# Optimization experiments

Hardware: AMD Instinct MI355X
Metric: run time of the kernel (lower is better)

The kernel has to match this reference:

```python
import jax, jax.numpy as jnp
import numpy as np

B, S, E, D, M = 512, 64, 768, 256, 3  # batch, seq, encoder_dim, dim, num_modalities


def setup_inputs() -> dict:
    key = jax.random.key(0)
    ks = jax.random.split(key, 16)
    inp = {}
    for i in range(M):
        inp[f"latent{i}"] = jax.random.normal(ks[i], (B, S, E), dtype=jnp.float32)
        inp[f"Wp{i}"] = jax.random.normal(ks[3 + i], (D, E), dtype=jnp.float32) * (1.0 / np.sqrt(E))
        inp[f"bp{i}"] = jnp.zeros((D,), dtype=jnp.float32)
    inp["corr"] = jax.random.uniform(ks[7], (D, D), dtype=jnp.float32, minval=-0.1, maxval=0.1)
    F_in = 2 * D * (M - 1)  # 1024
    inp["Wb"] = jax.random.normal(ks[8], (64, F_in), dtype=jnp.float32) * (1.0 / np.sqrt(F_in))
    inp["bb"] = jnp.zeros((64,), dtype=jnp.float32)
    inp["gamma"] = jnp.ones((64,), dtype=jnp.float32)
    inp["beta"] = jnp.zeros((64,), dtype=jnp.float32)
    return inp


def _forward(latents, Wps, bps, corr, Wb, bb, gamma, beta):
    # project each modality: [B,S,E] -> [B,S,D]
    proj = [lat @ Wp.T + bp for lat, Wp, bp in zip(latents, Wps, bps)]
    anchor = proj[0]
    pairs = []
    for other in proj[1:]:
        # cc[b,i,j] = anchor[b,i,:] @ corr @ other[b,j,:]
        cc = jnp.einsum('bid,de,bje->bij', anchor, corr, other)
        a_att = jax.nn.softmax(cc, axis=1)   # softmax over anchor tokens
        o_att = jax.nn.softmax(cc, axis=2)   # softmax over other tokens (= softmax(cc^T, dim=1))
        att_anchor = jnp.einsum('bid,bij->bdj', anchor, a_att) + jnp.swapaxes(anchor, 1, 2)
        att_other = jnp.einsum('bjd,bij->bdi', other, o_att) + jnp.swapaxes(other, 1, 2)
        pairs.append(jnp.concatenate([att_anchor, att_other], axis=1))  # [B,2D,S]
    fused = jnp.concatenate(pairs, axis=1)          # [B, 2D(M-1), S]
    fused = jnp.swapaxes(fused, 1, 2)               # [B, S, 2D(M-1)]
    h = fused @ Wb.T + bb                           # [B, S, 64]
    mu = jnp.mean(h, axis=-1, keepdims=True)
    var = jnp.var(h, axis=-1, keepdims=True)
    h = (h - mu) / jnp.sqrt(var + 1e-5) * gamma + beta
    return jax.nn.relu(h)


def reference(latent0, latent1, latent2, Wp0, bp0, Wp1, bp1, Wp2, bp2, corr, Wb, bb, gamma, beta):
    return _forward([latent0, latent1, latent2], [Wp0, Wp1, Wp2], [bp0, bp1, bp2],
                    corr, Wb, bb, gamma, beta)
```

## Files before the change

### kernel.cpp

```cpp
#include <hip/hip_runtime.h>
#include <hip/hip_bf16.h>
#include <stdint.h>

#define Bsz 512
#define Ssz 64
#define Esz 768
#define Dsz 256
#define MROWS (Bsz * Ssz)
#define FIN 1024

typedef _Float16 f16;
typedef f16 f16x4 __attribute__((ext_vector_type(4)));
typedef f16 f16x8v __attribute__((ext_vector_type(8)));
typedef float f32x4 __attribute__((ext_vector_type(4)));

__device__ __forceinline__ void async_copy16(const void* g, void* l) {
    __builtin_amdgcn_global_load_lds((const __attribute__((address_space(1))) uint32_t*)g,
                                     (__attribute__((address_space(3))) uint32_t*)l, 16, 0, 0);
}

__global__ __launch_bounds__(256) void prep(const float* __restrict__ Wp0,
                                            const float* __restrict__ Wp1,
                                            const float* __restrict__ Wp2,
                                            const float* __restrict__ corr,
                                            const float* __restrict__ Wb,
                                            f16* __restrict__ Wph,
                                            f16* __restrict__ corrT,
                                            f16* __restrict__ Wbh) {
    const int t = blockIdx.x * 256 + threadIdx.x;
    if (t < 3 * 196608) {
        const int z = t / 196608, i = t % 196608;
        const float* W = (z == 0) ? Wp0 : (z == 1) ? Wp1 : Wp2;
        Wph[(size_t)z * 196608 + i] = (f16)W[i];
    }
    if (t < 65536) {
        const int d = t >> 8, e = t & 255;
        corrT[e * 256 + d] = (f16)corr[d * 256 + e];
        Wbh[t] = (f16)Wb[t];
    }
}

template <bool A_F16, bool BIAS>
__global__ __launch_bounds__(256) void mfma_gemm(
    const float* __restrict__ A32a, const float* __restrict__ A32b,
    const float* __restrict__ A32c, const f16* __restrict__ A16,
    const f16* __restrict__ Bh, const float* __restrict__ biasA,
    const float* __restrict__ biasB, const float* __restrict__ biasC,
    f16* __restrict__ Ch, int K) {
    constexpr int ABYTES = A_F16 ? 8192 : 16384;
    constexpr int BUF = ABYTES + 8192;
    __shared__ __align__(16) char smem[2 * BUF];

    const int tid = threadIdx.x;
    const int n0 = blockIdx.x * 128;
    const int m0 = blockIdx.y * 128;
    const int z = blockIdx.z;
    const float* A32 = (z == 0) ? A32a : (z == 1) ? A32b : A32c;
    const float* bias = (z == 0) ? biasA : (z == 1) ? biasB : biasC;
    const f16* Bz = Bh + (size_t)z * 256 * K;
    f16* Cz = Ch + (size_t)z * MROWS * 256;

    const int lane = tid & 63;
    const int w = tid >> 6;
    const int lr = lane & 15;
    const int lk = lane >> 4;
    const int ma = (w >> 1) * 4;
    const int nb = (w & 1) * 4;

    f32x4 acc[4][4];
#pragma unroll
    for (int i = 0; i < 4; i++)
#pragma unroll
        for (int j = 0; j < 4; j++) acc[i][j] = (f32x4){0.f, 0.f, 0.f, 0.f};

    auto stage = [&](int buf, int k0) {
        char* base = smem + buf * BUF;
#pragma unroll
        for (int i = 0; i < (A_F16 ? 2 : 4); i++) {
            const int Ub = (w * (A_F16 ? 2 : 4) + i) * 64;
            const int U = Ub + lane;
            if constexpr (A_F16) {
                const int row = U >> 2, u = (U & 3) ^ (row & 3);
                async_copy16(A16 + (size_t)(m0 + row) * K + k0 + u * 8, base + Ub * 16);
            } else {
                const int row = U >> 3, c = (U & 7) ^ (row & 7);
                async_copy16(A32 + (size_t)(m0 + row) * K + k0 + c * 4, base + Ub * 16);
            }
        }
#pragma unroll
        for (int i = 0; i < 2; i++) {
            const int Ub = (w * 2 + i) * 64;
            const int U = Ub + lane;
            const int row = U >> 2, u = (U & 3) ^ (row & 3);
            async_copy16(Bz + (size_t)(n0 + row) * K + k0 + u * 8, base + ABYTES + Ub * 16);
        }
    };

    stage(0, 0);
    int cur = 0;
    const int NT = K >> 5;
    for (int t = 0; t < NT; t++) {
        if (t + 1 < NT) {
            stage(cur ^ 1, (t + 1) << 5);
            if constexpr (A_F16) {
                asm volatile("s_waitcnt vmcnt(4)" ::: "memory");
            } else {
                asm volatile("s_waitcnt vmcnt(6)" ::: "memory");
            }
        } else {
            asm volatile("s_waitcnt vmcnt(0)" ::: "memory");
        }
        __builtin_amdgcn_sched_barrier(0);
        asm volatile("s_barrier" ::: "memory");
        __builtin_amdgcn_sched_barrier(0);

        const char* base = smem + cur * BUF;
        const f16* Af16L = (const f16*)base;
        const float* Af32L = (const float*)base;
        const f16* BfL = (const f16*)(base + ABYTES);
        f16x8v af[4], bf[4];
#pragma unroll
        for (int i = 0; i < 4; i++) {
            const int row = (ma + i) * 16 + lr;
            if constexpr (A_F16) {
                const int u = lk ^ (row & 3);
                af[i] = *(const f16x8v*)&Af16L[(row * 4 + u) * 8];
            } else {
                const int c0 = (2 * lk) ^ (row & 7);
                const int c1 = (2 * lk + 1) ^ (row & 7);
                const float4 v1 = *(const float4*)&Af32L[(row * 8 + c0) * 4];
                const float4 v2 = *(const float4*)&Af32L[(row * 8 + c1) * 4];
                f16x8v h;
                h[0] = (f16)v1.x; h[1] = (f16)v1.y; h[2] = (f16)v1.z; h[3] = (f16)v1.w;
                h[4] = (f16)v2.x; h[5] = (f16)v2.y; h[6] = (f16)v2.z; h[7] = (f16)v2.w;
                af[i] = h;
            }
        }
#pragma unroll
        for (int j = 0; j < 4; j++) {
            const int row = (nb + j) * 16 + lr;
            const int u = lk ^ (row & 3);
            bf[j] = *(const f16x8v*)&BfL[(row * 4 + u) * 8];
        }
#pragma unroll
        for (int i = 0; i < 4; i++)
#pragma unroll
            for (int j = 0; j < 4; j++)
                acc[i][j] = __builtin_amdgcn_mfma_f32_16x16x32_f16(af[i], bf[j], acc[i][j], 0, 0, 0);

        __builtin_amdgcn_sched_barrier(0);
        asm volatile("s_barrier" ::: "memory");
        cur ^= 1;
    }

    f16* Ce = (f16*)smem;
    const int cr = lane & 15, qr = lane >> 4;
    const int mwl = (w >> 1) * 64;
    const int nwl = (w & 1) * 64;
#pragma unroll
    for (int i = 0; i < 4; i++) {
#pragma unroll
        for (int j = 0; j < 4; j++) {
            const int col = nwl + j * 16 + cr;
            const float bv = BIAS ? bias[n0 + col] : 0.f;
#pragma unroll
            for (int r = 0; r < 4; r++) {
                const int row = mwl + i * 16 + qr * 4 + r;
                Ce[row * 128 + col] = (f16)(acc[i][j][r] + bv);
            }
        }
    }
    __syncthreads();
#pragma unroll
    for (int r = 0; r < 8; r++) {
        const int f = r * 256 + tid;
        const int row = f >> 4, c16 = f & 15;
        uint4 v = *(const uint4*)&Ce[row * 128 + c16 * 8];
        *(uint4*)(Cz + (size_t)(m0 + row) * 256 + n0 + c16 * 8) = v;
    }
}

__global__ __launch_bounds__(256) void cc_softmax(const f16* __restrict__ ac,
                                                  const f16* __restrict__ proj1,
                                                  const f16* __restrict__ proj2,
                                                  f16* __restrict__ aT,
                                                  f16* __restrict__ oP) {
    const int b = blockIdx.x, q = blockIdx.y;
    const f16* __restrict__ A = ac + (size_t)b * Ssz * Dsz;
    const f16* __restrict__ Bp = (q ? proj2 : proj1) + (size_t)b * Ssz * Dsz;
    __shared__ float sc[64][65];
    __shared__ float pm[4][64], ps[4][64], qm[4][64], qs[4][64];
    __shared__ float CM[64], CI[64], RM[64], RI[64];
    const int tid = threadIdx.x;
    const int lane = tid & 63, w = tid >> 6;
    const int lr = lane & 15;
    const int lk = lane >> 4;

    f32x4 acc[4];
#pragma unroll
    for (int j = 0; j < 4; j++) acc[j] = (f32x4){0.f, 0.f, 0.f, 0.f};

    const f16* __restrict__ Arow = A + (size_t)(w * 16 + lr) * Dsz + lk * 8;
    for (int ks = 0; ks < 8; ks++) {
        f16x8v af = *(const f16x8v*)(Arow + ks * 32);
        f16x8v bf[4];
#pragma unroll
        for (int j = 0; j < 4; j++)
            bf[j] = *(const f16x8v*)(Bp + (size_t)(j * 16 + lr) * Dsz + ks * 32 + lk * 8);
#pragma unroll
        for (int j = 0; j < 4; j++)
            acc[j] = __builtin_amdgcn_mfma_f32_16x16x32_f16(af, bf[j], acc[j], 0, 0, 0);
    }
#pragma unroll
    for (int j = 0; j < 4; j++)
#pragma unroll
        for (int r = 0; r < 4; r++) sc[w * 16 + lk * 4 + r][j * 16 + lr] = acc[j][r];
    __syncthreads();

    const int lid = tid & 63, qa = tid >> 6;
    float m1 = -1e30f, m2 = -1e30f;
#pragma unroll
    for (int it = 0; it < 16; it++) {
        m1 = fmaxf(m1, sc[qa * 16 + it][lid]);
        m2 = fmaxf(m2, sc[lid][qa * 16 + it]);
    }
    float s1 = 0.f, s2 = 0.f;
#pragma unroll
    for (int it = 0; it < 16; it++) {
        s1 += __expf(sc[qa * 16 + it][lid] - m1);
        s2 += __expf(sc[lid][qa * 16 + it] - m2);
    }
    pm[qa][lid] = m1; ps[qa][lid] = s1;
    qm[qa][lid] = m2; qs[qa][lid] = s2;
    __syncthreads();
    if (tid < 128) {
        const int x = tid & 63;
        const bool col = tid < 64;
        float M = -1e30f;
#pragma unroll
        for (int u = 0; u < 4; u++) M = fmaxf(M, col ? pm[u][x] : qm[u][x]);
        float S = 0.f;
#pragma unroll
        for (int u = 0; u < 4; u++)
            S += (col ? ps[u][x] : qs[u][x]) * __expf((col ? pm[u][x] : qm[u][x]) - M);
        if (col) { CM[x] = M; CI[x] = 1.f / S; }
        else     { RM[x] = M; RI[x] = 1.f / S; }
    }
    __syncthreads();
    f16* __restrict__ apT = aT + (size_t)(q * Bsz + b) * 4096;
    f16* __restrict__ opR = oP + (size_t)(q * Bsz + b) * 4096;
#pragma unroll
    for (int it = 0; it < 16; it++) {
        const int i = qa * 16 + it;
        opR[i * 64 + lid] = (f16)(__expf(sc[i][lid] - RM[i]) * RI[i]);
        apT[i * 64 + lid] = (f16)(__expf(sc[lid][i] - CM[i]) * CI[i]);
    }
}

__global__ __launch_bounds__(256) void fused_tail(const f16* __restrict__ proj,
                                                  const f16* __restrict__ Wbh,
                                                  const f16* __restrict__ aT,
                                                  const f16* __restrict__ oP,
                                                  const float* __restrict__ bb,
                                                  const float* __restrict__ gamma,
                                                  const float* __restrict__ beta,
                                                  float* __restrict__ out) {
    const int b = blockIdx.x;
    const int tid = threadIdx.x, lane = tid & 63, w = tid >> 6;
    const int lr = lane & 15, lk = lane >> 4;

    __shared__ __align__(16) f16 Gs[4][4096];

    {
        const int q = w >> 1, part = w & 1;
        const int z = part ? (1 + q) : 0;
        const f16* __restrict__ X = proj + ((size_t)z * MROWS + b * 64) * 256;
        const f16* __restrict__ Wc = Wbh + q * 512 + part * 256;
        f32x4 gacc[4][4];
#pragma unroll
        for (int i = 0; i < 4; i++)
#pragma unroll
            for (int j = 0; j < 4; j++) gacc[i][j] = (f32x4){0.f, 0.f, 0.f, 0.f};
        for (int ks = 0; ks < 8; ks++) {
            f16x8v af[4], bf[4];
#pragma unroll
            for (int mi = 0; mi < 4; mi++)
                af[mi] = *(const f16x8v*)(Wc + (size_t)(mi * 16 + lr) * FIN + ks * 32 + lk * 8);
#pragma unroll
            for (int nj = 0; nj < 4; nj++)
                bf[nj] = *(const f16x8v*)(X + (size_t)(nj * 16 + lr) * 256 + ks * 32 + lk * 8);
#pragma unroll
            for (int mi = 0; mi < 4; mi++)
#pragma unroll
                for (int nj = 0; nj < 4; nj++)
                    gacc[mi][nj] = __builtin_amdgcn_mfma_f32_16x16x32_f16(af[mi], bf[nj], gacc[mi][nj], 0, 0, 0);
        }
#pragma unroll
        for (int mi = 0; mi < 4; mi++)
#pragma unroll
            for (int nj = 0; nj < 4; nj++)
#pragma unroll
                for (int r = 0; r < 4; r++) {
                    const int o = mi * 16 + lk * 4 + r;
                    const int t = nj * 16 + lr;
                    Gs[w][(o * 8 + ((t >> 3) ^ (o & 7))) * 8 + (t & 7)] = (f16)gacc[mi][nj][r];
                }
    }
    __syncthreads();

    f32x4 acc[4];
#pragma unroll
    for (int j = 0; j < 4; j++) acc[j] = (f32x4){0.f, 0.f, 0.f, 0.f};

#pragma unroll
    for (int term = 0; term < 4; term++) {
        const int q = term >> 1;
        const f16* __restrict__ Abase =
            ((term & 1) ? oP : aT) + ((size_t)(q * Bsz + b)) * 4096;
#pragma unroll
        for (int kh = 0; kh < 2; kh++) {
            f16x8v af = *(const f16x8v*)(Abase + (size_t)(w * 16 + lr) * 64 + kh * 32 + lk * 8);
#pragma unroll
            for (int jf = 0; jf < 4; jf++) {
                const int o = jf * 16 + lr;
                const int su = o * 8 + ((kh * 4 + lk) ^ (o & 7));
                f16x8v bf = *(const f16x8v*)&Gs[term][su * 8];
                acc[jf] = __builtin_amdgcn_mfma_f32_16x16x32_f16(af, bf, acc[jf], 0, 0, 0);
            }
        }
    }

    float bbv[4], gv[4], bv2[4];
#pragma unroll
    for (int jf = 0; jf < 4; jf++) {
        const int o = jf * 16 + lr;
        bbv[jf] = bb[o];
        gv[jf] = gamma[o];
        bv2[jf] = beta[o];
    }
#pragma unroll
    for (int r = 0; r < 4; r++) {
        const int s = w * 16 + lk * 4 + r;
        float h[4];
        float s1 = 0.f, s2 = 0.f;
#pragma unroll
        for (int jf = 0; jf < 4; jf++) {
            const int o = jf * 16 + lr;
            float resid = 0.f;
#pragma unroll
            for (int term = 0; term < 4; term++) {
                const int su = o * 8 + ((s >> 3) ^ (o & 7));
                resid += (float)Gs[term][su * 8 + (s & 7)];
            }
            h[jf] = acc[jf][r] + resid + bbv[jf];
            s1 += h[jf];
            s2 += h[jf] * h[jf];
        }
#pragma unroll
        for (int m = 1; m < 16; m <<= 1) {
            s1 += __shfl_xor(s1, m);
            s2 += __shfl_xor(s2, m);
        }
        const float mu = s1 * (1.f / 64.f);
        const float inv = rsqrtf(s2 * (1.f / 64.f) - mu * mu + 1e-5f);
#pragma unroll
        for (int jf = 0; jf < 4; jf++) {
            const float v = (h[jf] - mu) * inv * gv[jf] + bv2[jf];
            out[(size_t)(b * 64 + s) * 64 + jf * 16 + lr] = fmaxf(v, 0.f);
        }
    }
}

extern "C" void kernel_launch(void* const* d_in, const int* in_sizes, int n_in,
                              void* d_out, int out_size, void* d_ws, size_t ws_size,
                              hipStream_t stream) {
    const float* latent0 = (const float*)d_in[0];
    const float* Wp0 = (const float*)d_in[1];
    const float* bp0 = (const float*)d_in[2];
    const float* latent1 = (const float*)d_in[3];
    const float* Wp1 = (const float*)d_in[4];
    const float* bp1 = (const float*)d_in[5];
    const float* latent2 = (const float*)d_in[6];
    const float* Wp2 = (const float*)d_in[7];
    const float* bp2 = (const float*)d_in[8];
    const float* corr = (const float*)d_in[9];
    const float* Wb = (const float*)d_in[10];
    const float* bb = (const float*)d_in[11];
    const float* gamma = (const float*)d_in[12];
    const float* beta = (const float*)d_in[13];

    char* ws = (char*)d_ws;
    f16* proj_h = (f16*)ws;
    f16* ac_h = (f16*)(ws + 48ull * 1024 * 1024);
    f16* aT = (f16*)(ws + 64ull * 1024 * 1024);
    f16* oP = (f16*)(ws + 72ull * 1024 * 1024);
    f16* Wph = (f16*)(ws + 160ull * 1024 * 1024);
    f16* corrT = (f16*)(ws + 162ull * 1024 * 1024);
    f16* Wbh = (f16*)(ws + 162ull * 1024 * 1024 + 128ull * 1024);

    float* out = (float*)d_out;
    dim3 blk(256);

    prep<<<2304, blk, 0, stream>>>(Wp0, Wp1, Wp2, corr, Wb, Wph, corrT, Wbh);

    mfma_gemm<false, true><<<dim3(2, 256, 3), blk, 0, stream>>>(
        latent0, latent1, latent2, (const f16*)nullptr, Wph, bp0, bp1, bp2, proj_h, Esz);

    mfma_gemm<true, false><<<dim3(2, 256, 1), blk, 0, stream>>>(
        (const float*)nullptr, (const float*)nullptr, (const float*)nullptr, proj_h,
        corrT, (const float*)nullptr, (const float*)nullptr, (const float*)nullptr,
        ac_h, Dsz);

    const f16* proj1_h = proj_h + (size_t)MROWS * 256;
    const f16* proj2_h = proj_h + 2ull * MROWS * 256;

    cc_softmax<<<dim3(Bsz, 2), blk, 0, stream>>>(ac_h, proj1_h, proj2_h, aT, oP);

    fused_tail<<<Bsz, blk, 0, stream>>>(proj_h, Wbh, aT, oP, bb, gamma, beta, out);

    (void)in_sizes; (void)n_in; (void)out_size; (void)ws_size;
}
```

Measured before the change: 401.1 us.

## Widen GEMM tiles to full N, stage cc operands in LDS, vectorize tail stores

The projection and corr GEMMs now compute a 128x256 tile per block (full N), so the fp32 latent A-tile is loaded and converted once rather than twice, at the cost of double the accumulators and a 2-wave occupancy hint. The LDS swizzle gains an extra XOR term to reduce bank conflicts. cc_softmax copies its A and B operands into swizzled LDS asynchronously before the MFMA loop, instead of reading each fragment straight from global memory. fused_tail swaps the MFMA operand order so each lane can write its result as a packed 4-wide f16 store.

```diff
diff --git a/kernel.cpp b/kernel.cpp
--- a/kernel.cpp
+++ b/kernel.cpp
@@ -41,18 +41,18 @@
 }
 
 template <bool A_F16, bool BIAS>
-__global__ __launch_bounds__(256) void mfma_gemm(
+__global__ __launch_bounds__(256, 2) void mfma_gemm(
     const float* __restrict__ A32a, const float* __restrict__ A32b,
     const float* __restrict__ A32c, const f16* __restrict__ A16,
     const f16* __restrict__ Bh, const float* __restrict__ biasA,
     const float* __restrict__ biasB, const float* __restrict__ biasC,
     f16* __restrict__ Ch, int K) {
     constexpr int ABYTES = A_F16 ? 8192 : 16384;
-    constexpr int BUF = ABYTES + 8192;
-    __shared__ __align__(16) char smem[2 * BUF];
+    constexpr int BBYTES = 16384;
+    constexpr int BUF = ABYTES + BBYTES;
+    __shared__ __align__(16) char smem[65536];
 
     const int tid = threadIdx.x;
-    const int n0 = blockIdx.x * 128;
     const int m0 = blockIdx.y * 128;
     const int z = blockIdx.z;
     const float* A32 = (z == 0) ? A32a : (z == 1) ? A32b : A32c;
@@ -65,13 +65,13 @@
     const int lr = lane & 15;
     const int lk = lane >> 4;
     const int ma = (w >> 1) * 4;
-    const int nb = (w & 1) * 4;
-
-    f32x4 acc[4][4];
+    const int nb = (w & 1) * 8;
+
+    f32x4 acc[4][8];
 #pragma unroll
     for (int i = 0; i < 4; i++)
 #pragma unroll
-        for (int j = 0; j < 4; j++) acc[i][j] = (f32x4){0.f, 0.f, 0.f, 0.f};
+        for (int j = 0; j < 8; j++) acc[i][j] = (f32x4){0.f, 0.f, 0.f, 0.f};
 
     auto stage = [&](int buf, int k0) {
         char* base = smem + buf * BUF;
@@ -80,7 +80,7 @@
             const int Ub = (w * (A_F16 ? 2 : 4) + i) * 64;
             const int U = Ub + lane;
             if constexpr (A_F16) {
-                const int row = U >> 2, u = (U & 3) ^ (row & 3);
+                const int row = U >> 2, u = (U & 3) ^ (row & 3) ^ ((row >> 2) & 3);
                 async_copy16(A16 + (size_t)(m0 + row) * K + k0 + u * 8, base + Ub * 16);
             } else {
                 const int row = U >> 3, c = (U & 7) ^ (row & 7);
@@ -88,11 +88,11 @@
             }
         }
 #pragma unroll
-        for (int i = 0; i < 2; i++) {
-            const int Ub = (w * 2 + i) * 64;
+        for (int i = 0; i < 4; i++) {
+            const int Ub = (w * 4 + i) * 64;
             const int U = Ub + lane;
-            const int row = U >> 2, u = (U & 3) ^ (row & 3);
-            async_copy16(Bz + (size_t)(n0 + row) * K + k0 + u * 8, base + ABYTES + Ub * 16);
+            const int row = U >> 2, u = (U & 3) ^ (row & 3) ^ ((row >> 2) & 3);
+            async_copy16(Bz + (size_t)row * K + k0 + u * 8, base + ABYTES + Ub * 16);
         }
     };
 
@@ -103,9 +103,9 @@
         if (t + 1 < NT) {
             stage(cur ^ 1, (t + 1) << 5);
             if constexpr (A_F16) {
-                asm volatile("s_waitcnt vmcnt(4)" ::: "memory");
+                asm volatile("s_waitcnt vmcnt(6)" ::: "memory");
             } else {
-                asm volatile("s_waitcnt vmcnt(6)" ::: "memory");
+                asm volatile("s_waitcnt vmcnt(8)" ::: "memory");
             }
         } else {
             asm volatile("s_waitcnt vmcnt(0)" ::: "memory");
@@ -118,16 +118,16 @@
         const f16* Af16L = (const f16*)base;
         const float* Af32L = (const float*)base;
         const f16* BfL = (const f16*)(base + ABYTES);
-        f16x8v af[4], bf[4];
+        const int usw = lk ^ (lr & 3) ^ ((lr >> 2) & 3);
+        f16x8v af[4], bf[8];
 #pragma unroll
         for (int i = 0; i < 4; i++) {
             const int row = (ma + i) * 16 + lr;
             if constexpr (A_F16) {
-                const int u = lk ^ (row & 3);
-                af[i] = *(const f16x8v*)&Af16L[(row * 4 + u) * 8];
+                af[i] = *(const f16x8v*)&Af16L[(row * 4 + usw) * 8];
             } else {
-                const int c0 = (2 * lk) ^ (row & 7);
-                const int c1 = (2 * lk + 1) ^ (row & 7);
+                const int c0 = (2 * lk) ^ (lr & 7);
+                const int c1 = c0 ^ 1;
                 const float4 v1 = *(const float4*)&Af32L[(row * 8 + c0) * 4];
                 const float4 v2 = *(const float4*)&Af32L[(row * 8 + c1) * 4];
                 f16x8v h;
@@ -137,15 +137,14 @@
             }
         }
 #pragma unroll
-        for (int j = 0; j < 4; j++) {
+        for (int j = 0; j < 8; j++) {
             const int row = (nb + j) * 16 + lr;
-            const int u = lk ^ (row & 3);
-            bf[j] = *(const f16x8v*)&BfL[(row * 4 + u) * 8];
+            bf[j] = *(const f16x8v*)&BfL[(row * 4 + usw) * 8];
         }
 #pragma unroll
         for (int i = 0; i < 4; i++)
 #pragma unroll
-            for (int j = 0; j < 4; j++)
+            for (int j = 0; j < 8; j++)
                 acc[i][j] = __builtin_amdgcn_mfma_f32_16x16x32_f16(af[i], bf[j], acc[i][j], 0, 0, 0);
 
         __builtin_amdgcn_sched_barrier(0);
@@ -156,27 +155,27 @@
     f16* Ce = (f16*)smem;
     const int cr = lane & 15, qr = lane >> 4;
     const int mwl = (w >> 1) * 64;
-    const int nwl = (w & 1) * 64;
+    const int nwl = (w & 1) * 128;
 #pragma unroll
     for (int i = 0; i < 4; i++) {
 #pragma unroll
-        for (int j = 0; j < 4; j++) {
+        for (int j = 0; j < 8; j++) {
             const int col = nwl + j * 16 + cr;
-            const float bv = BIAS ? bias[n0 + col] : 0.f;
+            const float bv = BIAS ? bias[col] : 0.f;
 #pragma unroll
             for (int r = 0; r < 4; r++) {
                 const int row = mwl + i * 16 + qr * 4 + r;
-                Ce[row * 128 + col] = (f16)(acc[i][j][r] + bv);
-            }
-        }
-    }
-    __syncthreads();
-#pragma unroll
-    for (int r = 0; r < 8; r++) {
+                Ce[row * 256 + col] = (f16)(acc[i][j][r] + bv);
+            }
+        }
+    }
+    __syncthreads();
+#pragma unroll
+    for (int r = 0; r < 16; r++) {
         const int f = r * 256 + tid;
-        const int row = f >> 4, c16 = f & 15;
-        uint4 v = *(const uint4*)&Ce[row * 128 + c16 * 8];
-        *(uint4*)(Cz + (size_t)(m0 + row) * 256 + n0 + c16 * 8) = v;
+        const int row = f >> 5, c16 = f & 31;
+        uint4 v = *(const uint4*)&Ce[row * 256 + c16 * 8];
+        *(uint4*)(Cz + (size_t)(m0 + row) * 256 + c16 * 8) = v;
     }
 }
 
@@ -186,63 +185,88 @@
                                                   f16* __restrict__ aT,
                                                   f16* __restrict__ oP) {
     const int b = blockIdx.x, q = blockIdx.y;
-    const f16* __restrict__ A = ac + (size_t)b * Ssz * Dsz;
-    const f16* __restrict__ Bp = (q ? proj2 : proj1) + (size_t)b * Ssz * Dsz;
-    __shared__ float sc[64][65];
-    __shared__ float pm[4][64], ps[4][64], qm[4][64], qs[4][64];
-    __shared__ float CM[64], CI[64], RM[64], RI[64];
+    const f16* __restrict__ Ag = ac + (size_t)b * Ssz * Dsz;
+    const f16* __restrict__ Bg = (q ? proj2 : proj1) + (size_t)b * Ssz * Dsz;
+    __shared__ __align__(16) char csmem[65536];
+    f16* As = (f16*)csmem;
+    f16* Bs = (f16*)(csmem + 32768);
+    float* sc = (float*)csmem;
+    float* pm = (float*)(csmem + 32768);
+    float* ps = pm + 256;
+    float* qm = ps + 256;
+    float* qs = qm + 256;
+    float* CM = qs + 256;
+    float* CI = CM + 64;
+    float* RM = CI + 64;
+    float* RI = RM + 64;
+
     const int tid = threadIdx.x;
     const int lane = tid & 63, w = tid >> 6;
     const int lr = lane & 15;
     const int lk = lane >> 4;
 
+#pragma unroll
+    for (int r = 0; r < 8; r++) {
+        const int Ub = (w * 8 + r) * 64;
+        const int U = Ub + lane;
+        const int row = U >> 5, u0 = U & 31;
+        const int gu = u0 ^ (row & 15);
+        async_copy16(Ag + (size_t)row * 256 + gu * 8, csmem + Ub * 16);
+        async_copy16(Bg + (size_t)row * 256 + gu * 8, csmem + 32768 + Ub * 16);
+    }
+    __syncthreads();
+
     f32x4 acc[4];
 #pragma unroll
     for (int j = 0; j < 4; j++) acc[j] = (f32x4){0.f, 0.f, 0.f, 0.f};
 
-    const f16* __restrict__ Arow = A + (size_t)(w * 16 + lr) * Dsz + lk * 8;
     for (int ks = 0; ks < 8; ks++) {
-        f16x8v af = *(const f16x8v*)(Arow + ks * 32);
+        const int arow = w * 16 + lr;
+        f16x8v af = *(const f16x8v*)&As[(arow * 32 + ((ks * 4 + lk) ^ lr)) * 8];
         f16x8v bf[4];
 #pragma unroll
-        for (int j = 0; j < 4; j++)
-            bf[j] = *(const f16x8v*)(Bp + (size_t)(j * 16 + lr) * Dsz + ks * 32 + lk * 8);
+        for (int j = 0; j < 4; j++) {
+            const int brow = j * 16 + lr;
+            bf[j] = *(const f16x8v*)&Bs[(brow * 32 + ((ks * 4 + lk) ^ lr)) * 8];
+        }
 #pragma unroll
         for (int j = 0; j < 4; j++)
             acc[j] = __builtin_amdgcn_mfma_f32_16x16x32_f16(af, bf[j], acc[j], 0, 0, 0);
     }
+    __syncthreads();
 #pragma unroll
     for (int j = 0; j < 4; j++)
 #pragma unroll
-        for (int r = 0; r < 4; r++) sc[w * 16 + lk * 4 + r][j * 16 + lr] = acc[j][r];
+        for (int r = 0; r < 4; r++) sc[(w * 16 + lk * 4 + r) * 65 + j * 16 + lr] = acc[j][r];
     __syncthreads();
 
     const int lid = tid & 63, qa = tid >> 6;
     float m1 = -1e30f, m2 = -1e30f;
 #pragma unroll
     for (int it = 0; it < 16; it++) {
-        m1 = fmaxf(m1, sc[qa * 16 + it][lid]);
-        m2 = fmaxf(m2, sc[lid][qa * 16 + it]);
+        m1 = fmaxf(m1, sc[(qa * 16 + it) * 65 + lid]);
+        m2 = fmaxf(m2, sc[lid * 65 + qa * 16 + it]);
     }
     float s1 = 0.f, s2 = 0.f;
 #pragma unroll
     for (int it = 0; it < 16; it++) {
-        s1 += __expf(sc[qa * 16 + it][lid] - m1);
-        s2 += __expf(sc[lid][qa * 16 + it] - m2);
-    }
-    pm[qa][lid] = m1; ps[qa][lid] = s1;
-    qm[qa][lid] = m2; qs[qa][lid] = s2;
+        s1 += __expf(sc[(qa * 16 + it) * 65 + lid] - m1);
+        s2 += __expf(sc[lid * 65 + qa * 16 + it] - m2);
+    }
+    pm[qa * 64 + lid] = m1; ps[qa * 64 + lid] = s1;
+    qm[qa * 64 + lid] = m2; qs[qa * 64 + lid] = s2;
     __syncthreads();
     if (tid < 128) {
         const int x = tid & 63;
         const bool col = tid < 64;
         float M = -1e30f;
 #pragma unroll
-        for (int u = 0; u < 4; u++) M = fmaxf(M, col ? pm[u][x] : qm[u][x]);
+        for (int u = 0; u < 4; u++) M = fmaxf(M, col ? pm[u * 64 + x] : qm[u * 64 + x]);
         float S = 0.f;
 #pragma unroll
         for (int u = 0; u < 4; u++)
-            S += (col ? ps[u][x] : qs[u][x]) * __expf((col ? pm[u][x] : qm[u][x]) - M);
+            S += (col ? ps[u * 64 + x] : qs[u * 64 + x]) *
+                 __expf((col ? pm[u * 64 + x] : qm[u * 64 + x]) - M);
         if (col) { CM[x] = M; CI[x] = 1.f / S; }
         else     { RM[x] = M; RI[x] = 1.f / S; }
     }
@@ -252,8 +276,8 @@
 #pragma unroll
     for (int it = 0; it < 16; it++) {
         const int i = qa * 16 + it;
-        opR[i * 64 + lid] = (f16)(__expf(sc[i][lid] - RM[i]) * RI[i]);
-        apT[i * 64 + lid] = (f16)(__expf(sc[lid][i] - CM[i]) * CI[i]);
+        opR[i * 64 + lid] = (f16)(__expf(sc[i * 65 + lid] - RM[i]) * RI[i]);
+        apT[i * 64 + lid] = (f16)(__expf(sc[lid * 65 + i] - CM[i]) * CI[i]);
     }
 }
 
@@ -282,29 +306,32 @@
 #pragma unroll
             for (int j = 0; j < 4; j++) gacc[i][j] = (f32x4){0.f, 0.f, 0.f, 0.f};
         for (int ks = 0; ks < 8; ks++) {
-            f16x8v af[4], bf[4];
-#pragma unroll
-            for (int mi = 0; mi < 4; mi++)
-                af[mi] = *(const f16x8v*)(Wc + (size_t)(mi * 16 + lr) * FIN + ks * 32 + lk * 8);
-#pragma unroll
-            for (int nj = 0; nj < 4; nj++)
-                bf[nj] = *(const f16x8v*)(X + (size_t)(nj * 16 + lr) * 256 + ks * 32 + lk * 8);
-#pragma unroll
-            for (int mi = 0; mi < 4; mi++)
-#pragma unroll
-                for (int nj = 0; nj < 4; nj++)
-                    gacc[mi][nj] = __builtin_amdgcn_mfma_f32_16x16x32_f16(af[mi], bf[nj], gacc[mi][nj], 0, 0, 0);
-        }
-#pragma unroll
-        for (int mi = 0; mi < 4; mi++)
-#pragma unroll
-            for (int nj = 0; nj < 4; nj++)
-#pragma unroll
-                for (int r = 0; r < 4; r++) {
-                    const int o = mi * 16 + lk * 4 + r;
-                    const int t = nj * 16 + lr;
-                    Gs[w][(o * 8 + ((t >> 3) ^ (o & 7))) * 8 + (t & 7)] = (f16)gacc[mi][nj][r];
-                }
+            f16x8v xf[4], wf[4];
+#pragma unroll
+            for (int tt = 0; tt < 4; tt++)
+                xf[tt] = *(const f16x8v*)(X + (size_t)(tt * 16 + lr) * 256 + ks * 32 + lk * 8);
+#pragma unroll
+            for (int oo = 0; oo < 4; oo++)
+                wf[oo] = *(const f16x8v*)(Wc + (size_t)(oo * 16 + lr) * FIN + ks * 32 + lk * 8);
+#pragma unroll
+            for (int tt = 0; tt < 4; tt++)
+#pragma unroll
+                for (int oo = 0; oo < 4; oo++)
+                    gacc[tt][oo] = __builtin_amdgcn_mfma_f32_16x16x32_f16(xf[tt], wf[oo], gacc[tt][oo], 0, 0, 0);
+        }
+#pragma unroll
+        for (int tt = 0; tt < 4; tt++)
+#pragma unroll
+            for (int oo = 0; oo < 4; oo++) {
+                const int o = oo * 16 + lr;
+                const int su = o * 8 + ((tt * 2 + (lk >> 1)) ^ (o & 7));
+                f16x4 pk;
+                pk[0] = (f16)gacc[tt][oo][0];
+                pk[1] = (f16)gacc[tt][oo][1];
+                pk[2] = (f16)gacc[tt][oo][2];
+                pk[3] = (f16)gacc[tt][oo][3];
+                *(f16x4*)&Gs[w][su * 8 + (lk & 1) * 4] = pk;
+            }
     }
     __syncthreads();
 
@@ -403,10 +430,10 @@
 
     prep<<<2304, blk, 0, stream>>>(Wp0, Wp1, Wp2, corr, Wb, Wph, corrT, Wbh);
 
-    mfma_gemm<false, true><<<dim3(2, 256, 3), blk, 0, stream>>>(
+    mfma_gemm<false, true><<<dim3(1, 256, 3), blk, 0, stream>>>(
         latent0, latent1, latent2, (const f16*)nullptr, Wph, bp0, bp1, bp2, proj_h, Esz);
 
-    mfma_gemm<true, false><<<dim3(2, 256, 1), blk, 0, stream>>>(
+    mfma_gemm<true, false><<<dim3(1, 256, 1), blk, 0, stream>>>(
         (const float*)nullptr, (const float*)nullptr, (const float*)nullptr, proj_h,
         corrT, (const float*)nullptr, (const float*)nullptr, (const float*)nullptr,
         ac_h, Dsz);
```

Result: faster. 383.7 us (-4.3%).
